# Kernel optimization log

Hardware: AMD Instinct MI355X
Metric: run time of the kernel (lower is better)

Reference implementation:

```python
import jax, jax.numpy as jnp
import numpy as np

EPS = 1e-07
ITERS = 3
MEMBERS = 128  # membersPerGroup


def setup_inputs() -> dict:
    key = jax.random.key(0)
    k1, k2, k3 = jax.random.split(key, 3)
    B, H, W, C = 32, 48, 48, 512
    x = jax.random.normal(k1, (B, H, W, C), dtype=jnp.float32)
    gamma = jax.random.uniform(k2, (1, 1, 1, C), dtype=jnp.float32)
    beta = jax.random.normal(k3, (1, 1, 1, C), dtype=jnp.float32)
    return {"x": x, "gamma": gamma, "beta": beta}


def reference(x, gamma, beta):
    B, H, W, C = x.shape
    m = MEMBERS
    g = C // m
    N = B * H * W
    # flatten to (C, N), center with batch mean (training path)
    f = jnp.transpose(x, (3, 0, 1, 2)).reshape(C, N)
    mean = jnp.mean(f, axis=1, keepdims=True)
    f = f - mean
    fg = f.reshape(g, m, N)
    # per-group covariance, unbiased normalization (b*w*h - 1)
    cov = jnp.einsum('gmn,gkn->gmk', fg, fg) / (jnp.float32(N) - 1.0)
    eye = jnp.eye(m, dtype=jnp.float32)
    cov = (1.0 - EPS) * cov + EPS * eye[None]
    # Newton-Schulz inverse square root
    tr = jnp.einsum('gii->g', cov)[:, None, None]  # (g,1,1)
    sig = cov / tr
    P = jnp.broadcast_to(eye, (g, m, m))
    for _ in range(ITERS):
        P = (3.0 * P - P @ P @ P @ sig) / 2.0
    whiten = P / jnp.sqrt(tr)  # (g,m,m)
    # whiten features
    fhat = jnp.einsum('gmk,gkn->gmn', whiten, fg)  # (g,m,N)
    out = fhat.reshape(C, B, H, W).transpose(1, 2, 3, 0)
    return out * gamma + beta
```

## Files before the change

### kernel.cpp

```cpp
#include <hip/hip_runtime.h>
#include <hip/hip_bf16.h>
#include <cstdint>

#define NTOT 73728
#define CTOT 512
#define MGRP 128
#define EPSV 1e-7f

typedef float4 f4;
typedef __attribute__((ext_vector_type(8))) short bf16x8;
typedef __attribute__((ext_vector_type(4))) float f32x4;
typedef __attribute__((ext_vector_type(16))) float f32x16;

__device__ __forceinline__ f4 ld4(const float* p){ return *(const f4*)p; }

__device__ __forceinline__ ushort f2bf(float f){
    uint32_t u = __builtin_bit_cast(uint32_t, f);
    uint32_t r = (u + 0x7FFFu + ((u >> 16) & 1u)) >> 16;
    return (ushort)r;
}
__device__ __forceinline__ float bfval(ushort h){
    return __builtin_bit_cast(float, (uint32_t)h << 16);
}
__device__ __forceinline__ uint32_t pk2(float a, float b){
    __hip_bfloat162 h = __float22bfloat162_rn(make_float2(a, b));
    uint32_t u; __builtin_memcpy(&u, &h, 4);
    return u;
}
__device__ __forceinline__ bf16x8 pack8(const float v[8]) {
    union { bf16x8 b; uint32_t u[4]; } r;
#pragma unroll
    for (int i = 0; i < 4; ++i) r.u[i] = pk2(v[2*i], v[2*i+1]);
    return r.b;
}

__device__ __forceinline__ int mofs(int row, int col){
    return row * 128 + (((col >> 3) ^ (row & 15)) * 8) + (col & 7);
}
__device__ __forceinline__ bf16x8 mfrag(const ushort* M, int row, int ks, int h2){
    int slot = (ks * 2 + h2) ^ (row & 15);
    return *(const bf16x8*)&M[row * 128 + slot * 8];
}

__global__ __launch_bounds__(256) void k_cov(
    const float* __restrict__ x, float* __restrict__ sxxPart,
    float* __restrict__ sxPart, int nchunk, int rowsPer)
{
    const int chunk = blockIdx.x, g = blockIdx.y;
    const int t = threadIdx.x;
    const int lane = t & 63, wid = t >> 6;
    const int wr = wid >> 1, wc = wid & 1;
    const int l31 = lane & 31, hi = lane >> 5;
    const size_t rowbase = (size_t)chunk * rowsPer;

    __shared__ float xs[2][4096];
    __shared__ float sxred[256];

    const int kq0  = t >> 5;
    const int schk = t & 31;
    const float* xp = x + (size_t)g * MGRP + (size_t)schk * 4;
    const int wbase = kq0 * 512 + schk * 4;

    f32x16 acc[2][2];
#pragma unroll
    for (int a = 0; a < 2; ++a)
#pragma unroll
        for (int b = 0; b < 2; ++b) acc[a][b] = (f32x16){};
    float sxa0 = 0.f, sxa1 = 0.f;

    const int niter = rowsPer / 32;
    f4 r0 = ld4(xp + (rowbase + kq0*4 + 0) * CTOT);
    f4 r1 = ld4(xp + (rowbase + kq0*4 + 1) * CTOT);
    f4 r2 = ld4(xp + (rowbase + kq0*4 + 2) * CTOT);
    f4 r3 = ld4(xp + (rowbase + kq0*4 + 3) * CTOT);

    for (int it = 0; it < niter; ++it) {
        const int cur = it & 1;
        *(f32x4*)&xs[cur][wbase +   0] = (f32x4){r0.x, r1.x, r2.x, r3.x};
        *(f32x4*)&xs[cur][wbase + 128] = (f32x4){r0.y, r1.y, r2.y, r3.y};
        *(f32x4*)&xs[cur][wbase + 256] = (f32x4){r0.z, r1.z, r2.z, r3.z};
        *(f32x4*)&xs[cur][wbase + 384] = (f32x4){r0.w, r1.w, r2.w, r3.w};
        __syncthreads();
        if (it + 1 < niter) {
            const float* np = xp + (rowbase + (size_t)(it + 1) * 32 + kq0*4) * CTOT;
            r0 = ld4(np);
            r1 = ld4(np + CTOT);
            r2 = ld4(np + 2 * CTOT);
            r3 = ld4(np + 3 * CTOT);
        }
#pragma unroll
        for (int ks = 0; ks < 2; ++ks) {
            const int rbase = (ks*4 + hi*2) * 512 + (l31 >> 2) * 4 + (l31 & 3) * 128;
            bf16x8 fa[2], fb[2];
#pragma unroll
            for (int a = 0; a < 2; ++a) {
                const int ra = rbase + (wr*16 + a*8) * 4;
                f32x4 lo = *(const f32x4*)&xs[cur][ra];
                f32x4 hi4 = *(const f32x4*)&xs[cur][ra + 512];
                float v[8] = {lo.x, lo.y, lo.z, lo.w, hi4.x, hi4.y, hi4.z, hi4.w};
                if (wc == 0) {
                    float s = v[0]+v[1]+v[2]+v[3]+v[4]+v[5]+v[6]+v[7];
                    if (a == 0) sxa0 += s; else sxa1 += s;
                }
                fa[a] = pack8(v);
            }
            if (wr != wc) {
#pragma unroll
                for (int b = 0; b < 2; ++b) {
                    const int rb = rbase + (wc*16 + b*8) * 4;
                    f32x4 lo = *(const f32x4*)&xs[cur][rb];
                    f32x4 hi4 = *(const f32x4*)&xs[cur][rb + 512];
                    float v[8] = {lo.x, lo.y, lo.z, lo.w, hi4.x, hi4.y, hi4.z, hi4.w};
                    fb[b] = pack8(v);
                }
            } else {
                fb[0] = fa[0]; fb[1] = fa[1];
            }
#pragma unroll
            for (int a = 0; a < 2; ++a)
#pragma unroll
                for (int b = 0; b < 2; ++b)
                    acc[a][b] = __builtin_amdgcn_mfma_f32_32x32x16_bf16(
                        fa[a], fb[b], acc[a][b], 0, 0, 0);
        }
    }

    float* op = sxxPart + ((size_t)g * nchunk + chunk) * 16384;
#pragma unroll
    for (int a = 0; a < 2; ++a)
#pragma unroll
        for (int b = 0; b < 2; ++b)
#pragma unroll
            for (int r = 0; r < 16; ++r) {
                int i = wr*64 + a*32 + (r & 3) + 8 * (r >> 2) + 4 * hi;
                int j = wc*64 + b*32 + l31;
                op[i * 128 + j] = acc[a][b][r];
            }

    if (wc == 0) {
        sxred[(wr*64 + l31) * 2 + hi]      = sxa0;
        sxred[(wr*64 + 32 + l31) * 2 + hi] = sxa1;
    }
    __syncthreads();
    if (t < 128)
        sxPart[((size_t)g * nchunk + chunk) * 128 + t] = sxred[t*2] + sxred[t*2 + 1];
}

__global__ __launch_bounds__(256) void k_reduce(
    const float* __restrict__ sxxPart, float* __restrict__ gSxx, int nchunk)
{
    int g = blockIdx.y;
    int idx = blockIdx.x * 256 + threadIdx.x;
    float s = 0.f;
#pragma unroll 8
    for (int c = 0; c < nchunk; ++c)
        s += sxxPart[((size_t)g * nchunk + c) * 16384 + idx];
    gSxx[g * 16384 + idx] = s;
}

__global__ __launch_bounds__(256) void k_mid(
    const float* __restrict__ gSxx, const float* __restrict__ sxPart,
    const float* __restrict__ gamma, const float* __restrict__ beta,
    float* __restrict__ gBp, ushort* __restrict__ gWb, int nchunk)
{
    const int g = blockIdx.x;
    const int t = threadIdx.x;
    const int lane = t & 63, w = t >> 6;
    const int l31 = lane & 31, h2 = lane >> 5;

    __shared__ ushort Phi[16384], Plo[16384], Shi[16384], Thi[16384];
    __shared__ float muL[128];
    __shared__ float red[256];
    __shared__ float trS;

    {
        const int ch = t & 127, half = t >> 7;
        const int c0 = half * (nchunk >> 1), c1 = c0 + (nchunk >> 1);
        float s = 0.f;
#pragma unroll 8
        for (int c = c0; c < c1; ++c)
            s += sxPart[((size_t)g * nchunk + c) * 128 + ch];
        red[t] = s;
    }
    __syncthreads();
    if (t < 128) muL[t] = (red[t] + red[t + 128]) / (float)NTOT;
    __syncthreads();

    {
        float d = 0.f;
        if (t < 128) {
            float vdiag = gSxx[(size_t)g * 16384 + t * 128 + t];
            float cv = (vdiag - (float)NTOT * muL[t] * muL[t]) / ((float)NTOT - 1.f);
            d = (1.f - EPSV) * cv + EPSV;
        }
        red[t] = d;
        __syncthreads();
        for (int s = 128; s > 0; s >>= 1) {
            if (t < s) red[t] += red[t + s];
            __syncthreads();
        }
        if (t == 0) trS = red[0];
    }
    __syncthreads();

    const float invTr = 1.f / trS;
#pragma unroll 8
    for (int e = t; e < 16384; e += 256) {
        int i = e >> 7, j = e & 127;
        float cv = (gSxx[(size_t)g * 16384 + e] - (float)NTOT * muL[i] * muL[j]) / ((float)NTOT - 1.f);
        float ce = (1.f - EPSV) * cv + ((i == j) ? EPSV : 0.f);
        float sg = ce * invTr;
        Shi[mofs(i, j)] = f2bf(sg);
        float p0 = ((i == j) ? 1.5f : 0.f) - 0.5f * sg;
        ushort ph = f2bf(p0);
        Phi[mofs(i, j)] = ph;
        Plo[mofs(i, j)] = f2bf(p0 - bfval(ph));
    }
    __syncthreads();

    const int arow = 32 * w + l31;
#pragma unroll 1
    for (int it = 0; it < 2; ++it) {
        f32x16 t1[4];
#pragma unroll
        for (int ct = 0; ct < 4; ++ct) t1[ct] = (f32x16){};
#pragma unroll
        for (int ks = 0; ks < 8; ++ks) {
            bf16x8 ah = mfrag(Phi, arow, ks, h2);
            bf16x8 al = mfrag(Plo, arow, ks, h2);
#pragma unroll
            for (int ct = 0; ct < 4; ++ct) {
                bf16x8 bh = mfrag(Phi, ct*32 + l31, ks, h2);
                bf16x8 bl = mfrag(Plo, ct*32 + l31, ks, h2);
                t1[ct] = __builtin_amdgcn_mfma_f32_32x32x16_bf16(ah, bh, t1[ct], 0, 0, 0);
                t1[ct] = __builtin_amdgcn_mfma_f32_32x32x16_bf16(ah, bl, t1[ct], 0, 0, 0);
                t1[ct] = __builtin_amdgcn_mfma_f32_32x32x16_bf16(al, bh, t1[ct], 0, 0, 0);
            }
        }
        __syncthreads();
#pragma unroll
        for (int ct = 0; ct < 4; ++ct)
#pragma unroll
            for (int r = 0; r < 16; ++r) {
                int row = 32*w + (r & 3) + 8*(r >> 2) + 4*h2;
                Thi[mofs(row, ct*32 + l31)] = f2bf(t1[ct][r]);
            }
        __syncthreads();
        f32x16 t2[4];
#pragma unroll
        for (int ct = 0; ct < 4; ++ct) t2[ct] = (f32x16){};
#pragma unroll
        for (int ks = 0; ks < 8; ++ks) {
            bf16x8 ah = mfrag(Thi, arow, ks, h2);
#pragma unroll
            for (int ct = 0; ct < 4; ++ct) {
                bf16x8 bh = mfrag(Phi, ct*32 + l31, ks, h2);
                bf16x8 bl = mfrag(Plo, ct*32 + l31, ks, h2);
                t2[ct] = __builtin_amdgcn_mfma_f32_32x32x16_bf16(ah, bh, t2[ct], 0, 0, 0);
                t2[ct] = __builtin_amdgcn_mfma_f32_32x32x16_bf16(ah, bl, t2[ct], 0, 0, 0);
            }
        }
        __syncthreads();
#pragma unroll
        for (int ct = 0; ct < 4; ++ct)
#pragma unroll
            for (int r = 0; r < 16; ++r) {
                int row = 32*w + (r & 3) + 8*(r >> 2) + 4*h2;
                Thi[mofs(row, ct*32 + l31)] = f2bf(t2[ct][r]);
            }
        __syncthreads();
        f32x16 t3[4];
#pragma unroll
        for (int ct = 0; ct < 4; ++ct) t3[ct] = (f32x16){};
#pragma unroll
        for (int ks = 0; ks < 8; ++ks) {
            bf16x8 ah = mfrag(Thi, arow, ks, h2);
#pragma unroll
            for (int ct = 0; ct < 4; ++ct) {
                bf16x8 bh = mfrag(Shi, ct*32 + l31, ks, h2);
                t3[ct] = __builtin_amdgcn_mfma_f32_32x32x16_bf16(ah, bh, t3[ct], 0, 0, 0);
            }
        }
        __syncthreads();
#pragma unroll
        for (int ct = 0; ct < 4; ++ct)
#pragma unroll
            for (int r = 0; r < 16; ++r) {
                int row = 32*w + (r & 3) + 8*(r >> 2) + 4*h2;
                int o = mofs(row, ct*32 + l31);
                float pold = bfval(Phi[o]) + bfval(Plo[o]);
                float pnew = 1.5f * pold - 0.5f * t3[ct][r];
                ushort ph = f2bf(pnew);
                Phi[o] = ph;
                Plo[o] = f2bf(pnew - bfval(ph));
            }
        __syncthreads();
    }

    const float scale = rsqrtf(trS);
    {
        const int row = t & 127, half = t >> 7;
        float s = 0.f;
#pragma unroll 8
        for (int k = half * 64; k < half * 64 + 64; ++k) {
            int o = mofs(row, k);
            s += muL[k] * (bfval(Phi[o]) + bfval(Plo[o]));
        }
        red[t] = s;
    }
    __syncthreads();
    if (t < 128) {
        float s = (red[t] + red[t + 128]) * scale;
        int c = g * 128 + t;
        gBp[c] = beta[c] - gamma[c] * s;
    }
#pragma unroll 4
    for (int e2 = t; e2 < 8192; e2 += 256) {
        int row = e2 >> 6, cp = (e2 & 63) * 2;
        float sg = scale * gamma[g * 128 + row];
        int o0 = mofs(row, cp), o1 = mofs(row, cp + 1);
        float v0 = (bfval(Phi[o0]) + bfval(Plo[o0])) * sg;
        float v1 = (bfval(Phi[o1]) + bfval(Plo[o1])) * sg;
        *(uint32_t*)&gWb[(size_t)g * 16384 + row * 128 + cp] = pk2(v0, v1);
    }
}

__global__ __launch_bounds__(256) void k_apply(
    const float* __restrict__ x, const ushort* __restrict__ gWb,
    const float* __restrict__ gBp, float* __restrict__ out)
{
    const int g = blockIdx.y;
    const int t = threadIdx.x, lane = t & 63, w = t >> 6;
    const int l31 = lane & 31, hi = lane >> 5;

    __shared__ ushort Wl[16384];

    {
        const uint4* src = (const uint4*)(gWb + (size_t)g * 16384);
#pragma unroll
        for (int q = 0; q < 8; ++q) {
            int i = q * 256 + t;
            int row = i >> 4, s = i & 15;
            uint4 v = src[i];
            *(uint4*)&Wl[row * 128 + ((s ^ (row & 15)) * 8)] = v;
        }
    }
    __syncthreads();

    float bp[4];
#pragma unroll
    for (int ct = 0; ct < 4; ++ct)
        bp[ct] = gBp[g * MGRP + ct * 32 + l31];

    const int base = (blockIdx.x * 4 + w) * 64;
    const float* ap = x + (size_t)(base + l31) * CTOT + g * MGRP + hi * 8;

    f4 st0[8], st1[8];
#pragma unroll
    for (int ks = 0; ks < 8; ++ks) {
        st0[ks] = ld4(ap + ks * 16);
        st1[ks] = ld4(ap + ks * 16 + 4);
    }

#pragma unroll
    for (int tile = 0; tile < 2; ++tile) {
        bf16x8 af[8];
#pragma unroll
        for (int ks = 0; ks < 8; ++ks) {
            union { bf16x8 b; uint32_t u[4]; } cv;
            cv.u[0] = pk2(st0[ks].x, st0[ks].y);
            cv.u[1] = pk2(st0[ks].z, st0[ks].w);
            cv.u[2] = pk2(st1[ks].x, st1[ks].y);
            cv.u[3] = pk2(st1[ks].z, st1[ks].w);
            af[ks] = cv.b;
        }
        if (tile < 1) {
            const float* np = ap + (size_t)32 * CTOT;
#pragma unroll
            for (int ks = 0; ks < 8; ++ks) {
                st0[ks] = ld4(np + ks * 16);
                st1[ks] = ld4(np + ks * 16 + 4);
            }
        }
        const int s0 = base + tile * 32;
#pragma unroll
        for (int ct = 0; ct < 4; ++ct) {
            const int row = ct * 32 + l31;
            f32x16 acc = {};
#pragma unroll
            for (int ks = 0; ks < 8; ++ks) {
                int slot = (ks * 2 + hi) ^ (row & 15);
                bf16x8 wf = *(const bf16x8*)&Wl[row * 128 + slot * 8];
                acc = __builtin_amdgcn_mfma_f32_32x32x16_bf16(af[ks], wf, acc, 0, 0, 0);
            }
#pragma unroll
            for (int r = 0; r < 16; ++r) {
                int orow = s0 + (r & 3) + 8 * (r >> 2) + 4 * hi;
                float val = acc[r] + bp[ct];
                __builtin_nontemporal_store(val,
                    &out[(size_t)orow * CTOT + g * MGRP + ct * 32 + l31]);
            }
        }
    }
}

extern "C" void kernel_launch(void* const* d_in, const int* in_sizes, int n_in,
                              void* d_out, int out_size, void* d_ws, size_t ws_size,
                              hipStream_t stream)
{
    const float* x     = (const float*)d_in[0];
    const float* gamma = (const float*)d_in[1];
    const float* beta  = (const float*)d_in[2];
    float* out = (float*)d_out;
    float* ws  = (float*)d_ws;

    int nchunk = 128;
    auto need = [](int nc) -> size_t {
        return ((size_t)nc * 4 * 16384 + (size_t)nc * 4 * 128 +
                4 * 16384 + 512 + 32768) * 4;
    };
    while (nchunk > 16 && need(nchunk) > ws_size) nchunk >>= 1;
    int rowsPer = NTOT / nchunk;

    size_t off = 0;
    float* sxxPart = ws + off; off += (size_t)nchunk * 4 * 16384;
    float* sxPart  = ws + off; off += (size_t)nchunk * 4 * 128;
    float* gSxx    = ws + off; off += 4 * 16384;
    float* gBp     = ws + off; off += 512;
    ushort* gWb    = (ushort*)(ws + off); off += 32768;

    k_cov<<<dim3(nchunk, 4), 256, 0, stream>>>(x, sxxPart, sxPart, nchunk, rowsPer);
    k_reduce<<<dim3(64, 4), 256, 0, stream>>>(sxxPart, gSxx, nchunk);
    k_mid<<<4, 256, 0, stream>>>(gSxx, sxPart, gamma, beta, gBp, gWb, nchunk);
    k_apply<<<dim3(288, 4), 256, 0, stream>>>(x, gWb, gBp, out);
}
```

Baseline: 131.1 us.

## Split covariance kernel across 8 waves with one 32-column tile per wave

Doubles the k_cov block from 4 to 8 waves. Each wave now owns a 64x32 output tile instead of 64x64, and each thread loads two rows instead of four. The aim is more parallelism and latency hiding for the global loads and MFMA chain. In exchange it drops the symmetric-tile shortcut where diagonal waves reused the A fragments as B, so there is more redundant LDS reading and bf16 packing, plus a heavier barrier.

```diff
diff --git a/kernel.cpp b/kernel.cpp
--- a/kernel.cpp
+++ b/kernel.cpp
@@ -9,6 +9,7 @@
 
 typedef float4 f4;
 typedef __attribute__((ext_vector_type(8))) short bf16x8;
+typedef __attribute__((ext_vector_type(2))) float f32x2;
 typedef __attribute__((ext_vector_type(4))) float f32x4;
 typedef __attribute__((ext_vector_type(16))) float f32x16;
 
@@ -42,86 +43,76 @@
     return *(const bf16x8*)&M[row * 128 + slot * 8];
 }
 
-__global__ __launch_bounds__(256) void k_cov(
+__global__ __launch_bounds__(512) void k_cov(
     const float* __restrict__ x, float* __restrict__ sxxPart,
     float* __restrict__ sxPart, int nchunk, int rowsPer)
 {
     const int chunk = blockIdx.x, g = blockIdx.y;
     const int t = threadIdx.x;
     const int lane = t & 63, wid = t >> 6;
-    const int wr = wid >> 1, wc = wid & 1;
+    const int wr = wid >> 2, wc = wid & 3;
     const int l31 = lane & 31, hi = lane >> 5;
     const size_t rowbase = (size_t)chunk * rowsPer;
 
     __shared__ float xs[2][4096];
     __shared__ float sxred[256];
 
-    const int kq0  = t >> 5;
     const int schk = t & 31;
+    const int kq   = (t >> 5) & 7;
+    const int h    = t >> 8;
     const float* xp = x + (size_t)g * MGRP + (size_t)schk * 4;
-    const int wbase = kq0 * 512 + schk * 4;
-
-    f32x16 acc[2][2];
-#pragma unroll
-    for (int a = 0; a < 2; ++a)
-#pragma unroll
-        for (int b = 0; b < 2; ++b) acc[a][b] = (f32x16){};
+    const int wbase = kq * 512 + schk * 4 + 2 * h;
+
+    f32x16 acc[2];
+#pragma unroll
+    for (int a = 0; a < 2; ++a) acc[a] = (f32x16){};
     float sxa0 = 0.f, sxa1 = 0.f;
 
     const int niter = rowsPer / 32;
-    f4 r0 = ld4(xp + (rowbase + kq0*4 + 0) * CTOT);
-    f4 r1 = ld4(xp + (rowbase + kq0*4 + 1) * CTOT);
-    f4 r2 = ld4(xp + (rowbase + kq0*4 + 2) * CTOT);
-    f4 r3 = ld4(xp + (rowbase + kq0*4 + 3) * CTOT);
+    const int s0 = kq * 4 + 2 * h;
+    f4 r0 = ld4(xp + (rowbase + s0) * CTOT);
+    f4 r1 = ld4(xp + (rowbase + s0 + 1) * CTOT);
 
     for (int it = 0; it < niter; ++it) {
         const int cur = it & 1;
-        *(f32x4*)&xs[cur][wbase +   0] = (f32x4){r0.x, r1.x, r2.x, r3.x};
-        *(f32x4*)&xs[cur][wbase + 128] = (f32x4){r0.y, r1.y, r2.y, r3.y};
-        *(f32x4*)&xs[cur][wbase + 256] = (f32x4){r0.z, r1.z, r2.z, r3.z};
-        *(f32x4*)&xs[cur][wbase + 384] = (f32x4){r0.w, r1.w, r2.w, r3.w};
+        *(f32x2*)&xs[cur][wbase +   0] = (f32x2){r0.x, r1.x};
+        *(f32x2*)&xs[cur][wbase + 128] = (f32x2){r0.y, r1.y};
+        *(f32x2*)&xs[cur][wbase + 256] = (f32x2){r0.z, r1.z};
+        *(f32x2*)&xs[cur][wbase + 384] = (f32x2){r0.w, r1.w};
         __syncthreads();
         if (it + 1 < niter) {
-            const float* np = xp + (rowbase + (size_t)(it + 1) * 32 + kq0*4) * CTOT;
+            const float* np = xp + (rowbase + (size_t)(it + 1) * 32 + s0) * CTOT;
             r0 = ld4(np);
             r1 = ld4(np + CTOT);
-            r2 = ld4(np + 2 * CTOT);
-            r3 = ld4(np + 3 * CTOT);
         }
 #pragma unroll
         for (int ks = 0; ks < 2; ++ks) {
             const int rbase = (ks*4 + hi*2) * 512 + (l31 >> 2) * 4 + (l31 & 3) * 128;
-            bf16x8 fa[2], fb[2];
+            bf16x8 fa[2], fb;
+            float va[2][8];
 #pragma unroll
             for (int a = 0; a < 2; ++a) {
                 const int ra = rbase + (wr*16 + a*8) * 4;
-                f32x4 lo = *(const f32x4*)&xs[cur][ra];
+                f32x4 lo  = *(const f32x4*)&xs[cur][ra];
                 f32x4 hi4 = *(const f32x4*)&xs[cur][ra + 512];
+                va[a][0]=lo.x; va[a][1]=lo.y; va[a][2]=lo.z; va[a][3]=lo.w;
+                va[a][4]=hi4.x; va[a][5]=hi4.y; va[a][6]=hi4.z; va[a][7]=hi4.w;
+                fa[a] = pack8(va[a]);
+            }
+            if (wc == 0) {
+                sxa0 += va[0][0]+va[0][1]+va[0][2]+va[0][3]+va[0][4]+va[0][5]+va[0][6]+va[0][7];
+                sxa1 += va[1][0]+va[1][1]+va[1][2]+va[1][3]+va[1][4]+va[1][5]+va[1][6]+va[1][7];
+            }
+            {
+                const int rb = rbase + (wc*8) * 4;
+                f32x4 lo  = *(const f32x4*)&xs[cur][rb];
+                f32x4 hi4 = *(const f32x4*)&xs[cur][rb + 512];
                 float v[8] = {lo.x, lo.y, lo.z, lo.w, hi4.x, hi4.y, hi4.z, hi4.w};
-                if (wc == 0) {
-                    float s = v[0]+v[1]+v[2]+v[3]+v[4]+v[5]+v[6]+v[7];
-                    if (a == 0) sxa0 += s; else sxa1 += s;
-                }
-                fa[a] = pack8(v);
-            }
-            if (wr != wc) {
-#pragma unroll
-                for (int b = 0; b < 2; ++b) {
-                    const int rb = rbase + (wc*16 + b*8) * 4;
-                    f32x4 lo = *(const f32x4*)&xs[cur][rb];
-                    f32x4 hi4 = *(const f32x4*)&xs[cur][rb + 512];
-                    float v[8] = {lo.x, lo.y, lo.z, lo.w, hi4.x, hi4.y, hi4.z, hi4.w};
-                    fb[b] = pack8(v);
-                }
-            } else {
-                fb[0] = fa[0]; fb[1] = fa[1];
+                fb = pack8(v);
             }
 #pragma unroll
             for (int a = 0; a < 2; ++a)
-#pragma unroll
-                for (int b = 0; b < 2; ++b)
-                    acc[a][b] = __builtin_amdgcn_mfma_f32_32x32x16_bf16(
-                        fa[a], fb[b], acc[a][b], 0, 0, 0);
+                acc[a] = __builtin_amdgcn_mfma_f32_32x32x16_bf16(fa[a], fb, acc[a], 0, 0, 0);
         }
     }
 
@@ -129,13 +120,11 @@
 #pragma unroll
     for (int a = 0; a < 2; ++a)
 #pragma unroll
-        for (int b = 0; b < 2; ++b)
-#pragma unroll
-            for (int r = 0; r < 16; ++r) {
-                int i = wr*64 + a*32 + (r & 3) + 8 * (r >> 2) + 4 * hi;
-                int j = wc*64 + b*32 + l31;
-                op[i * 128 + j] = acc[a][b][r];
-            }
+        for (int r = 0; r < 16; ++r) {
+            int i = wr*64 + a*32 + (r & 3) + 8 * (r >> 2) + 4 * hi;
+            int j = wc*32 + l31;
+            op[i * 128 + j] = acc[a][r];
+        }
 
     if (wc == 0) {
         sxred[(wr*64 + l31) * 2 + hi]      = sxa0;
@@ -429,7 +418,7 @@
     float* gBp     = ws + off; off += 512;
     ushort* gWb    = (ushort*)(ws + off); off += 32768;
 
-    k_cov<<<dim3(nchunk, 4), 256, 0, stream>>>(x, sxxPart, sxPart, nchunk, rowsPer);
+    k_cov<<<dim3(nchunk, 4), 512, 0, stream>>>(x, sxxPart, sxPart, nchunk, rowsPer);
     k_reduce<<<dim3(64, 4), 256, 0, stream>>>(sxxPart, gSxx, nchunk);
     k_mid<<<4, 256, 0, stream>>>(gSxx, sxPart, gamma, beta, gBp, gWb, nchunk);
     k_apply<<<dim3(288, 4), 256, 0, stream>>>(x, gWb, gBp, out);
```

Measured after the change: 141.3 us. 7.8% more time.
